# Performance work log

Hardware: AMD Instinct MI355X
Metric: run time of the kernel (lower is better)

The kernel has to match this reference:

```python
import jax, jax.numpy as jnp
import numpy as np

S, B, T, D, NUM_CH = 16, 64, 640, 256, 4
T_WAV = 1.0 / 16000.0
LOG_F_MEAN = 5.02654
LOG_F_STD = 0.373288


def _make_i_2pi(output_dim, num_channels):
    num_freq = output_dim // num_channels
    # harmonic index i+1 repeated num_channels times, times 2*pi -> (D, 1)
    i_vec = np.repeat(np.arange(1, num_freq + 1, dtype=np.float32), num_channels)
    return jnp.asarray(i_vec * (2.0 * np.pi)).reshape(output_dim, 1)


def _make_k_T(time_len):
    # sample times 0..T-1 scaled by 1/16000 -> (1, T)
    return (jnp.arange(time_len, dtype=jnp.float32) * T_WAV).reshape(1, time_len)


def setup_inputs() -> dict:
    key = jax.random.key(0)
    k1, k2, k3, k4, k5 = jax.random.split(key, 5)
    x = jax.random.normal(k1, (S, B, 1, T), dtype=jnp.float32)
    nlf = jax.random.normal(k2, (S, B, 1, 1), dtype=jnp.float32)
    tau = jax.random.uniform(k3, (S, B, 1, 1), dtype=jnp.float32) * (T * T_WAV)
    a = jax.random.normal(k4, (D, 1), dtype=jnp.float32)
    phi = jax.random.normal(k5, (D, 1), dtype=jnp.float32)
    return {"x": x, "nlf": nlf, "tau": tau, "a": a, "phi": phi,
            "i_2pi": _make_i_2pi(D, NUM_CH), "k_T": _make_k_T(T)}


def reference(x, nlf, tau, a, phi, i_2pi, k_T):
    # f: denormalized fundamental frequency, (S,B,1,1)
    f = jnp.exp(nlf * LOG_F_STD + LOG_F_MEAN)
    # t: shifted time axis, (S,B,1,T)
    t = k_T - tau
    # deg = i*2pi*f*t + phi -> (S,B,D,T)
    i_f = i_2pi * f            # (S,B,D,1)
    deg = i_f * t + phi        # (S,B,D,T)
    W = a * jnp.sin(deg)       # (S,B,D,T)
    h_SBDT = W * x             # (S,B,D,T)  <- the huge intermediate
    return jnp.sum(h_SBDT, axis=-1)  # (S,B,D)
```

## Files before the change

kernel.cpp:

```cpp
#include <hip/hip_runtime.h>

constexpr int S_ = 16;
constexpr int B_ = 64;
constexpr int T_ = 640;
constexpr int D_ = 256;
constexpr int H_ = 64;

__device__ __forceinline__ float fractf_(float x) { return __builtin_amdgcn_fractf(x); }
__device__ __forceinline__ float sin2pi_(float r) { return __builtin_amdgcn_sinf(r); }

__global__ __launch_bounds__(256, 4)
void sinenet_kernel(const float* __restrict__ x,
                    const float* __restrict__ nlf,
                    const float* __restrict__ tau,
                    const float* __restrict__ a,
                    const float* __restrict__ phi,
                    float* __restrict__ out)
{
    __shared__ __align__(16) float xs[T_];
    __shared__ float redS[4][H_];
    __shared__ float redC[4][H_];

    const int sb   = blockIdx.x;
    const int tid  = threadIdx.x;
    const int w    = tid >> 6;
    const int lane = tid & 63;

    const float4* xg4 = reinterpret_cast<const float4*>(x + (size_t)sb * T_);
    if (tid < T_ / 4) reinterpret_cast<float4*>(xs)[tid] = xg4[tid];

    const double fd = exp((double)nlf[sb] * 0.373288 + 5.02654);
    const double g  = fd * (1.0 / 16000.0);
    const double q  = fd * (double)tau[sb];

    const int kstart = w * 160;

    const double hp = (double)(lane + 1);
    double mu = hp * g;
    mu -= floor(mu);
    double r0 = mu * (double)kstart - hp * q;
    r0 -= floor(r0);

    const float muf  = (float)mu;
    const float r0f  = (float)r0;
    const float sm   = sin2pi_(fractf_(muf));
    const float cm   = sin2pi_(fractf_(muf + 0.25f));
    float s          = sin2pi_(fractf_(r0f));
    float c          = sin2pi_(fractf_(r0f + 0.25f));

    float Ss = 0.0f, Cs = 0.0f;

    __syncthreads();

    const float4* xl = reinterpret_cast<const float4*>(xs + kstart);
#pragma unroll 4
    for (int i = 0; i < 40; ++i) {
        const float4 xv = xl[i];

        Ss = fmaf(s, xv.x, Ss); Cs = fmaf(c, xv.x, Cs);
        { float ns = fmaf(s, cm, c * sm); c = fmaf(c, cm, -(s * sm)); s = ns; }

        Ss = fmaf(s, xv.y, Ss); Cs = fmaf(c, xv.y, Cs);
        { float ns = fmaf(s, cm, c * sm); c = fmaf(c, cm, -(s * sm)); s = ns; }

        Ss = fmaf(s, xv.z, Ss); Cs = fmaf(c, xv.z, Cs);
        { float ns = fmaf(s, cm, c * sm); c = fmaf(c, cm, -(s * sm)); s = ns; }

        Ss = fmaf(s, xv.w, Ss); Cs = fmaf(c, xv.w, Cs);
        { float ns = fmaf(s, cm, c * sm); c = fmaf(c, cm, -(s * sm)); s = ns; }
    }

    redS[w][lane] = Ss;
    redC[w][lane] = Cs;
    __syncthreads();

    const int d = tid;
    const int h = tid >> 2;
    const float Sh = redS[0][h] + redS[1][h] + redS[2][h] + redS[3][h];
    const float Ch = redC[0][h] + redC[1][h] + redC[2][h] + redC[3][h];

    const float av  = a[d];
    const float pr  = phi[d] * 0.15915494309189535f;
    const float sp  = sin2pi_(fractf_(pr));
    const float cp  = sin2pi_(fractf_(pr + 0.25f));

    out[(size_t)sb * D_ + d] = av * fmaf(cp, Sh, sp * Ch);
}

extern "C" void kernel_launch(void* const* d_in, const int* in_sizes, int n_in,
                              void* d_out, int out_size, void* d_ws, size_t ws_size,
                              hipStream_t stream)
{
    const float* x   = (const float*)d_in[0];
    const float* nlf = (const float*)d_in[1];
    const float* tau = (const float*)d_in[2];
    const float* a   = (const float*)d_in[3];
    const float* phi = (const float*)d_in[4];
    float* out = (float*)d_out;

    dim3 grid(S_ * B_);
    dim3 block(256);
    hipLaunchKernelGGL(sinenet_kernel, grid, block, 0, stream,
                       x, nlf, tau, a, phi, out);
}
```

Before: 71.63 us.

## Split rotation into two independent chains and precompute per-row constants in prologue kernel

Each thread now runs two independent sine/cosine rotation recurrences over two halves of its 160-sample span, so the serial FMA dependency chain is half as long and there is more instruction-level parallelism. A new small pre-kernel computes the per-(s,b) double-precision exp and scaling terms and the per-d a·sin/cos(phi) coefficients once, and writes them to workspace. The main kernel reads these instead of recomputing the double exp and the phi sines in every block. This adds a second kernel launch and a dependency through the workspace, and uses more registers for the doubled chain state.

After: 71.45 us. Within noise of the previous version (-0.2%).

```diff
diff --git a/kernel.cpp b/kernel.cpp
--- a/kernel.cpp
+++ b/kernel.cpp
@@ -1,21 +1,47 @@
 #include <hip/hip_runtime.h>
 
-constexpr int S_ = 16;
-constexpr int B_ = 64;
-constexpr int T_ = 640;
-constexpr int D_ = 256;
-constexpr int H_ = 64;
+constexpr int S_  = 16;
+constexpr int B_  = 64;
+constexpr int T_  = 640;
+constexpr int D_  = 256;
+constexpr int H_  = 64;
+constexpr int SB_ = S_ * B_;
 
 __device__ __forceinline__ float fractf_(float x) { return __builtin_amdgcn_fractf(x); }
 __device__ __forceinline__ float sin2pi_(float r) { return __builtin_amdgcn_sinf(r); }
 
+struct GQ { double g, q; };
+
+__global__ void sinenet_pre(const float* __restrict__ nlf,
+                            const float* __restrict__ tau,
+                            const float* __restrict__ a,
+                            const float* __restrict__ phi,
+                            GQ* __restrict__ gq,
+                            float* __restrict__ ca,
+                            float* __restrict__ sa)
+{
+    const int idx = blockIdx.x * 256 + threadIdx.x;
+    if (idx < SB_) {
+        const double fd = exp((double)nlf[idx] * 0.373288 + 5.02654);
+        GQ v;
+        v.g = fd * (1.0 / 16000.0);
+        v.q = fd * (double)tau[idx];
+        gq[idx] = v;
+    } else if (idx < SB_ + D_) {
+        const int d  = idx - SB_;
+        const float av = a[d];
+        const float pr = phi[d] * 0.15915494309189535f;
+        sa[d] = av * sin2pi_(fractf_(pr));
+        ca[d] = av * sin2pi_(fractf_(pr + 0.25f));
+    }
+}
+
 __global__ __launch_bounds__(256, 4)
-void sinenet_kernel(const float* __restrict__ x,
-                    const float* __restrict__ nlf,
-                    const float* __restrict__ tau,
-                    const float* __restrict__ a,
-                    const float* __restrict__ phi,
-                    float* __restrict__ out)
+void sinenet_main(const float* __restrict__ x,
+                  const GQ* __restrict__ gq,
+                  const float* __restrict__ ca,
+                  const float* __restrict__ sa,
+                  float* __restrict__ out)
 {
     __shared__ __align__(16) float xs[T_];
     __shared__ float redS[4][H_];
@@ -29,62 +55,57 @@
     const float4* xg4 = reinterpret_cast<const float4*>(x + (size_t)sb * T_);
     if (tid < T_ / 4) reinterpret_cast<float4*>(xs)[tid] = xg4[tid];
 
-    const double fd = exp((double)nlf[sb] * 0.373288 + 5.02654);
-    const double g  = fd * (1.0 / 16000.0);
-    const double q  = fd * (double)tau[sb];
+    const double g = gq[sb].g;
+    const double q = gq[sb].q;
 
-    const int kstart = w * 160;
+    const int kA = w * 160;
+    const int kB = kA + 80;
 
     const double hp = (double)(lane + 1);
-    double mu = hp * g;
-    mu -= floor(mu);
-    double r0 = mu * (double)kstart - hp * q;
-    r0 -= floor(r0);
+    double mu = hp * g;  mu -= floor(mu);
+    double rA = mu * (double)kA - hp * q;  rA -= floor(rA);
+    double rB = rA + mu * 80.0;            rB -= floor(rB);
 
-    const float muf  = (float)mu;
-    const float r0f  = (float)r0;
-    const float sm   = sin2pi_(fractf_(muf));
-    const float cm   = sin2pi_(fractf_(muf + 0.25f));
-    float s          = sin2pi_(fractf_(r0f));
-    float c          = sin2pi_(fractf_(r0f + 0.25f));
+    const float muf = (float)mu;
+    const float sm  = sin2pi_(fractf_(muf));
+    const float cm  = sin2pi_(fractf_(muf + 0.25f));
+    float sA = sin2pi_(fractf_((float)rA));
+    float cA = sin2pi_(fractf_((float)rA + 0.25f));
+    float sB = sin2pi_(fractf_((float)rB));
+    float cB = sin2pi_(fractf_((float)rB + 0.25f));
 
-    float Ss = 0.0f, Cs = 0.0f;
+    float SsA = 0.0f, CsA = 0.0f, SsB = 0.0f, CsB = 0.0f;
 
     __syncthreads();
 
-    const float4* xl = reinterpret_cast<const float4*>(xs + kstart);
+    const float4* xa = reinterpret_cast<const float4*>(xs + kA);
+    const float4* xb = reinterpret_cast<const float4*>(xs + kB);
+
+#define STEP(sv, cv, Sacc, Cacc, xval)                                  \
+    Sacc = fmaf(sv, xval, Sacc); Cacc = fmaf(cv, xval, Cacc);           \
+    { float ns_ = fmaf(sv, cm, cv * sm);                                \
+      cv = fmaf(cv, cm, -(sv * sm)); sv = ns_; }
+
 #pragma unroll 4
-    for (int i = 0; i < 40; ++i) {
-        const float4 xv = xl[i];
+    for (int i = 0; i < 20; ++i) {
+        const float4 va = xa[i];
+        const float4 vb = xb[i];
+        STEP(sA, cA, SsA, CsA, va.x)  STEP(sB, cB, SsB, CsB, vb.x)
+        STEP(sA, cA, SsA, CsA, va.y)  STEP(sB, cB, SsB, CsB, vb.y)
+        STEP(sA, cA, SsA, CsA, va.z)  STEP(sB, cB, SsB, CsB, vb.z)
+        STEP(sA, cA, SsA, CsA, va.w)  STEP(sB, cB, SsB, CsB, vb.w)
+    }
+#undef STEP
 
-        Ss = fmaf(s, xv.x, Ss); Cs = fmaf(c, xv.x, Cs);
-        { float ns = fmaf(s, cm, c * sm); c = fmaf(c, cm, -(s * sm)); s = ns; }
-
-        Ss = fmaf(s, xv.y, Ss); Cs = fmaf(c, xv.y, Cs);
-        { float ns = fmaf(s, cm, c * sm); c = fmaf(c, cm, -(s * sm)); s = ns; }
-
-        Ss = fmaf(s, xv.z, Ss); Cs = fmaf(c, xv.z, Cs);
-        { float ns = fmaf(s, cm, c * sm); c = fmaf(c, cm, -(s * sm)); s = ns; }
-
-        Ss = fmaf(s, xv.w, Ss); Cs = fmaf(c, xv.w, Cs);
-        { float ns = fmaf(s, cm, c * sm); c = fmaf(c, cm, -(s * sm)); s = ns; }
-    }
-
-    redS[w][lane] = Ss;
-    redC[w][lane] = Cs;
+    redS[w][lane] = SsA + SsB;
+    redC[w][lane] = CsA + CsB;
     __syncthreads();
 
     const int d = tid;
     const int h = tid >> 2;
     const float Sh = redS[0][h] + redS[1][h] + redS[2][h] + redS[3][h];
     const float Ch = redC[0][h] + redC[1][h] + redC[2][h] + redC[3][h];
-
-    const float av  = a[d];
-    const float pr  = phi[d] * 0.15915494309189535f;
-    const float sp  = sin2pi_(fractf_(pr));
-    const float cp  = sin2pi_(fractf_(pr + 0.25f));
-
-    out[(size_t)sb * D_ + d] = av * fmaf(cp, Sh, sp * Ch);
+    out[(size_t)sb * D_ + d] = fmaf(ca[d], Sh, sa[d] * Ch);
 }
 
 extern "C" void kernel_launch(void* const* d_in, const int* in_sizes, int n_in,
@@ -98,8 +119,12 @@
     const float* phi = (const float*)d_in[4];
     float* out = (float*)d_out;
 
-    dim3 grid(S_ * B_);
-    dim3 block(256);
-    hipLaunchKernelGGL(sinenet_kernel, grid, block, 0, stream,
-                       x, nlf, tau, a, phi, out);
+    GQ*    gq = (GQ*)d_ws;
+    float* ca = (float*)((char*)d_ws + SB_ * sizeof(GQ));
+    float* sa = ca + D_;
+
+    hipLaunchKernelGGL(sinenet_pre, dim3((SB_ + D_ + 255) / 256), dim3(256), 0, stream,
+                       nlf, tau, a, phi, gq, ca, sa);
+    hipLaunchKernelGGL(sinenet_main, dim3(SB_), dim3(256), 0, stream,
+                       x, gq, ca, sa, out);
 }
```
